# Kernel tuning notes

Measured on AMD Instinct MI355X. Metric: run time of the kernel, lower is better.

Reference implementation:

```python
import jax, jax.numpy as jnp
import numpy as np

DIM = 192
HEADS = 16
DIM_HEAD = 64
INNER = HEADS * DIM_HEAD  # 1024
B, N = 8, 1024


def setup_inputs() -> dict:
    key = jax.random.key(0)
    ks = jax.random.split(key, 8)
    x = jax.random.normal(ks[0], (B, N, DIM), dtype=jnp.float32)
    shift = jax.random.normal(ks[1], (B, 1, DIM), dtype=jnp.float32)
    scale = jax.random.normal(ks[2], (B, 1, DIM), dtype=jnp.float32)
    norm_w = jnp.ones((DIM,), dtype=jnp.float32)
    norm_b = jnp.zeros((DIM,), dtype=jnp.float32)
    w_qkv = jax.random.normal(ks[3], (DIM, 3 * INNER), dtype=jnp.float32) * (DIM ** -0.5)
    w_out = jax.random.normal(ks[4], (INNER, DIM), dtype=jnp.float32) * (INNER ** -0.5)
    b_out = jnp.zeros((DIM,), dtype=jnp.float32)
    return {"x": x, "shift": shift, "scale": scale, "norm_w": norm_w,
            "norm_b": norm_b, "w_qkv": w_qkv, "w_out": w_out, "b_out": b_out}


def _layernorm(x, w, b, eps=1e-5):
    mu = jnp.mean(x, axis=-1, keepdims=True)
    var = jnp.mean(jnp.square(x - mu), axis=-1, keepdims=True)
    return (x - mu) * jax.lax.rsqrt(var + eps) * w + b


def reference(x, shift, scale, norm_w, norm_b, w_qkv, w_out, b_out):
    h = _layernorm(x, norm_w, norm_b)
    h = h * (1.0 + scale) + shift  # adaLN modulation, broadcast over tokens
    qkv = h @ w_qkv  # [B, N, 3*INNER]
    q, k, v = jnp.split(qkv, 3, axis=-1)
    # [B, N, INNER] -> [B, H, N, Dh]
    def split_heads(t):
        return t.reshape(B, N, HEADS, DIM_HEAD).transpose(0, 2, 1, 3)
    q, k, v = split_heads(q), split_heads(k), split_heads(v)
    scores = jnp.einsum('bhnd,bhmd->bhnm', q, k) * (DIM_HEAD ** -0.5)
    attn = jax.nn.softmax(scores, axis=-1)
    out = jnp.einsum('bhnm,bhmd->bhnd', attn, v)  # [B, H, N, Dh]
    out = out.transpose(0, 2, 1, 3).reshape(B, N, INNER)
    return out @ w_out + b_out
```

## Files before the change

kernel.cpp:

```cpp
#include <hip/hip_runtime.h>

#define DIM 192
#define NB 8
#define NTOK 1024
#define HEADS 16
#define DH 64
#define INNER 1024
#define ROWS (NB * NTOK)

typedef __bf16 bf16x8 __attribute__((ext_vector_type(8)));
typedef float f32x4 __attribute__((ext_vector_type(4)));
typedef float f32x16 __attribute__((ext_vector_type(16)));
typedef unsigned int u32x4 __attribute__((ext_vector_type(4)));

__device__ inline unsigned short f2bf(float f) {
    union { float f; unsigned u; } v; v.f = f;
    unsigned r = v.u + 0x7FFF + ((v.u >> 16) & 1);
    return (unsigned short)(r >> 16);
}

__device__ inline unsigned pk2(float a, float b) {
    __bf16 x = (__bf16)a, y = (__bf16)b;
    unsigned short ux = __builtin_bit_cast(unsigned short, x);
    unsigned short uy = __builtin_bit_cast(unsigned short, y);
    return (unsigned)ux | ((unsigned)uy << 16);
}

__device__ inline size_t fragIdx(int row, int k, int depth) {
    return ((size_t)(row >> 5) * ((size_t)depth * 4) +
            (size_t)(((k >> 4) * 2 + ((k >> 3) & 1)) * 32 + (row & 31))) * 8 + (k & 7);
}

__global__ __launch_bounds__(256) void k_pre(
    const float* __restrict__ x, const float* __restrict__ shift,
    const float* __restrict__ scale, const float* __restrict__ nw,
    const float* __restrict__ nb, const float* __restrict__ wqkv,
    const float* __restrict__ wout,
    unsigned short* __restrict__ hF, unsigned short* __restrict__ wF,
    unsigned short* __restrict__ woF) {
    int bid = blockIdx.x;
    if (bid < 2048) {
        int row = bid * 4 + (threadIdx.x >> 6);
        int lane = threadIdx.x & 63;
        const float* xr = x + row * DIM;
        float v0 = xr[lane], v1 = xr[lane + 64], v2 = xr[lane + 128];
        float s = v0 + v1 + v2;
        #pragma unroll
        for (int m = 1; m < 64; m <<= 1) s += __shfl_xor(s, m);
        float mean = s * (1.0f / DIM);
        float d0 = v0 - mean, d1 = v1 - mean, d2 = v2 - mean;
        float q = d0 * d0 + d1 * d1 + d2 * d2;
        #pragma unroll
        for (int m = 1; m < 64; m <<= 1) q += __shfl_xor(q, m);
        float rs = rsqrtf(q * (1.0f / DIM) + 1e-5f);
        int b = row >> 10;
        float vv[3] = {v0, v1, v2};
        #pragma unroll
        for (int i = 0; i < 3; i++) {
            int d = lane + 64 * i;
            float val = (vv[i] - mean) * rs * nw[d] + nb[d];
            val = val * (1.0f + scale[b * DIM + d]) + shift[b * DIM + d];
            hF[fragIdx(row, d, DIM)] = f2bf(val);
        }
    } else if (bid < 4352) {
        int idx = (bid - 2048) * 256 + threadIdx.x;
        int k = idx / 3072, c = idx % 3072;
        wF[fragIdx(c, k, DIM)] = f2bf(wqkv[idx]);
    } else {
        int idx = (bid - 4352) * 256 + threadIdx.x;
        int k = idx / 192, c = idx % 192;
        woF[fragIdx(c, k, INNER)] = f2bf(wout[idx]);
    }
}

__global__ __launch_bounds__(256, 3) void k_qkv(
    const unsigned short* __restrict__ hF, const unsigned short* __restrict__ wF,
    unsigned short* __restrict__ qmF, unsigned short* __restrict__ kmF,
    unsigned short* __restrict__ vtF) {
    const float QSC = 0.125f * 1.4426950408889634f;
    int tid = threadIdx.x;
    int wave = tid >> 6, lane = tid & 63;
    int l31 = lane & 31, hi = lane >> 5;
    int c0 = blockIdx.x * 64 + (wave >> 1) * 32;
    int typ = c0 >> 10;
    int hd  = (c0 & 1023) >> 6;
    int coff = c0 & 32;

    const unsigned short* Ab = wF + (size_t)(c0 >> 5) * 768 * 8;
    bf16x8 af[12];
    #pragma unroll
    for (int kc = 0; kc < 12; kc++)
        af[kc] = *(const bf16x8*)(Ab + ((kc * 2 + hi) * 32 + l31) * 8);

    #pragma unroll
    for (int ns = 0; ns < 2; ns++) {
        int n0 = blockIdx.y * 128 + (wave & 1) * 64 + ns * 32;
        const unsigned short* Bb = hF + (size_t)(n0 >> 5) * 768 * 8;
        f32x16 acc0, acc1;
        #pragma unroll
        for (int r = 0; r < 16; r++) { acc0[r] = 0.f; acc1[r] = 0.f; }
        if (typ < 2) {
            #pragma unroll
            for (int kc = 0; kc < 6; kc++) {
                bf16x8 bf0 = *(const bf16x8*)(Bb + (((2 * kc) * 2 + hi) * 32 + l31) * 8);
                bf16x8 bf1 = *(const bf16x8*)(Bb + (((2 * kc + 1) * 2 + hi) * 32 + l31) * 8);
                acc0 = __builtin_amdgcn_mfma_f32_32x32x16_bf16(af[2 * kc], bf0, acc0, 0, 0, 0);
                acc1 = __builtin_amdgcn_mfma_f32_32x32x16_bf16(af[2 * kc + 1], bf1, acc1, 0, 0, 0);
            }
        } else {
            #pragma unroll
            for (int kc = 0; kc < 6; kc++) {
                bf16x8 bf0 = *(const bf16x8*)(Bb + (((2 * kc) * 2 + hi) * 32 + l31) * 8);
                bf16x8 bf1 = *(const bf16x8*)(Bb + (((2 * kc + 1) * 2 + hi) * 32 + l31) * 8);
                acc0 = __builtin_amdgcn_mfma_f32_32x32x16_bf16(bf0, af[2 * kc], acc0, 0, 0, 0);
                acc1 = __builtin_amdgcn_mfma_f32_32x32x16_bf16(bf1, af[2 * kc + 1], acc1, 0, 0, 0);
            }
        }
        f32x16 acc;
        #pragma unroll
        for (int r = 0; r < 16; r++) acc[r] = acc0[r] + acc1[r];

        int bb = n0 >> 10, nm = n0 & 1023;
        int tt = nm >> 6;
        unsigned short* base;
        if (typ == 0) base = qmF + (size_t)(bb * 16 + hd) * 65536;
        else if (typ == 1) base = kmF + (size_t)(bb * 16 + hd) * 65536;
        else base = vtF + (size_t)(bb * 16 + hd) * 65536;

        if (typ < 2) {
            float sc = (typ == 0) ? QSC : 1.0f;
            int rowgrp = (nm >> 5) & 1;
            #pragma unroll
            for (int rg = 0; rg < 4; rg++) {
                int ob = coff + rg * 8;
                int g = (rowgrp * 4 + (ob >> 4)) * 2 + ((ob >> 3) & 1);
                uint2 val;
                val.x = pk2(acc[rg * 4 + 0] * sc, acc[rg * 4 + 1] * sc);
                val.y = pk2(acc[rg * 4 + 2] * sc, acc[rg * 4 + 3] * sc);
                *(uint2*)(base + (tt * 16 + g) * 256 + l31 * 8 + hi * 4) = val;
            }
        } else {
            int drg = coff >> 5;
            #pragma unroll
            for (int rg = 0; rg < 4; rg++) {
                int nb2 = (nm & 32) + rg * 8;
                int g = (drg * 4 + (nb2 >> 4)) * 2 + ((nb2 >> 3) & 1);
                uint2 val;
                val.x = pk2(acc[rg * 4 + 0], acc[rg * 4 + 1]);
                val.y = pk2(acc[rg * 4 + 2], acc[rg * 4 + 3]);
                *(uint2*)(base + (tt * 16 + g) * 256 + l31 * 8 + hi * 4) = val;
            }
        }
    }
}

__global__ __launch_bounds__(256, 3) void k_attn(
    const unsigned short* __restrict__ qmF, const unsigned short* __restrict__ kmF,
    const unsigned short* __restrict__ vtF, unsigned short* __restrict__ attnF) {
    int tid = threadIdx.x;
    int wave = tid >> 6, lane = tid & 63;
    int l31 = lane & 31, hi = lane >> 5;
    int bh = blockIdx.x, qt = blockIdx.y;
    int qbase = qt * 128 + wave * 32;
    const unsigned short* Qb = qmF + (size_t)bh * 65536;
    const unsigned short* Kb = kmF + (size_t)bh * 65536;
    const unsigned short* Vb = vtF + (size_t)bh * 65536;

    int tq = qbase >> 6, rq = (qbase >> 5) & 1;
    bf16x8 qf[4];
    #pragma unroll
    for (int c = 0; c < 4; c++)
        qf[c] = *(const bf16x8*)(Qb + (tq * 16 + (rq * 4 + c) * 2 + hi) * 256 + l31 * 8);

    float lsum = 0.f;
    f32x16 accO[2];
    #pragma unroll
    for (int r = 0; r < 16; r++) { accO[0][r] = 0.f; accO[1][r] = 0.f; }

    auto ldKf = [&](int t, int rowgrp, int c) -> bf16x8 {
        return *(const bf16x8*)(Kb + (t * 16 + (rowgrp * 4 + c) * 2 + hi) * 256 + l31 * 8);
    };
    auto ldVf = [&](int t, int dt, int nc) -> bf16x8 {
        return *(const bf16x8*)(Vb + (t * 16 + (dt * 4 + nc) * 2 + hi) * 256 + l31 * 8);
    };
    auto packP = [&](const f32x16& P, bf16x8& w0, bf16x8& w1) {
        u32x4 A, B;
        {
            auto r0 = __builtin_amdgcn_permlane32_swap(pk2(P[0], P[1]), pk2(P[4], P[5]), false, false);
            auto r1 = __builtin_amdgcn_permlane32_swap(pk2(P[2], P[3]), pk2(P[6], P[7]), false, false);
            A[0] = r0[0]; A[1] = r1[0]; A[2] = r0[1]; A[3] = r1[1];
        }
        {
            auto r0 = __builtin_amdgcn_permlane32_swap(pk2(P[8], P[9]), pk2(P[12], P[13]), false, false);
            auto r1 = __builtin_amdgcn_permlane32_swap(pk2(P[10], P[11]), pk2(P[14], P[15]), false, false);
            B[0] = r0[0]; B[1] = r1[0]; B[2] = r0[1]; B[3] = r1[1];
        }
        w0 = __builtin_bit_cast(bf16x8, A);
        w1 = __builtin_bit_cast(bf16x8, B);
    };
    auto tsum = [](const f32x16& P) -> float {
        float s0 = (P[0] + P[1]) + (P[2] + P[3]);
        float s1 = (P[4] + P[5]) + (P[6] + P[7]);
        float s2 = (P[8] + P[9]) + (P[10] + P[11]);
        float s3 = (P[12] + P[13]) + (P[14] + P[15]);
        return (s0 + s1) + (s2 + s3);
    };

    bf16x8 pw[4];

    {
        f32x16 C0, C1;
        #pragma unroll
        for (int r = 0; r < 16; r++) { C0[r] = 0.f; C1[r] = 0.f; }
        #pragma unroll
        for (int c = 0; c < 4; c++) {
            C0 = __builtin_amdgcn_mfma_f32_32x32x16_bf16(ldKf(0, 0, c), qf[c], C0, 0, 0, 0);
            C1 = __builtin_amdgcn_mfma_f32_32x32x16_bf16(ldKf(0, 1, c), qf[c], C1, 0, 0, 0);
        }
        #pragma unroll
        for (int r = 0; r < 16; r++) {
            C0[r] = __builtin_amdgcn_exp2f(C0[r]);
            C1[r] = __builtin_amdgcn_exp2f(C1[r]);
        }
        lsum += tsum(C0) + tsum(C1);
        packP(C0, pw[0], pw[1]);
        packP(C1, pw[2], pw[3]);
    }

    for (int t = 1; t < 16; t++) {
        f32x16 C0, C1;
        #pragma unroll
        for (int r = 0; r < 16; r++) { C0[r] = 0.f; C1[r] = 0.f; }
        #pragma unroll
        for (int c = 0; c < 4; c++) {
            C0 = __builtin_amdgcn_mfma_f32_32x32x16_bf16(ldKf(t, 0, c), qf[c], C0, 0, 0, 0);
            C1 = __builtin_amdgcn_mfma_f32_32x32x16_bf16(ldKf(t, 1, c), qf[c], C1, 0, 0, 0);
        }
        #pragma unroll
        for (int dt = 0; dt < 2; dt++) {
            #pragma unroll
            for (int nc = 0; nc < 4; nc++) {
                accO[dt] = __builtin_amdgcn_mfma_f32_32x32x16_bf16(
                    ldVf(t - 1, dt, nc), pw[nc], accO[dt], 0, 0, 0);
            }
        }

        #pragma unroll
        for (int r = 0; r < 16; r++) {
            C0[r] = __builtin_amdgcn_exp2f(C0[r]);
            C1[r] = __builtin_amdgcn_exp2f(C1[r]);
        }
        lsum += tsum(C0) + tsum(C1);
        packP(C0, pw[0], pw[1]);
        packP(C1, pw[2], pw[3]);
    }

    #pragma unroll
    for (int dt = 0; dt < 2; dt++) {
        #pragma unroll
        for (int nc = 0; nc < 4; nc++) {
            accO[dt] = __builtin_amdgcn_mfma_f32_32x32x16_bf16(
                ldVf(15, dt, nc), pw[nc], accO[dt], 0, 0, 0);
        }
    }

    float inv = 1.0f / (lsum + __shfl_xor(lsum, 32));
    int b = bh >> 4, hd = bh & 15;
    int rowblk = b * 32 + qt * 4 + wave;
    #pragma unroll
    for (int dt = 0; dt < 2; dt++)
        #pragma unroll
        for (int rg = 0; rg < 4; rg++) {
            int g = (hd * 4 + dt * 2 + (rg >> 1)) * 2 + (rg & 1);
            uint2 val;
            val.x = pk2(accO[dt][rg * 4 + 0] * inv, accO[dt][rg * 4 + 1] * inv);
            val.y = pk2(accO[dt][rg * 4 + 2] * inv, accO[dt][rg * 4 + 3] * inv);
            *(uint2*)((char*)attnF + ((size_t)rowblk * 4096 + g * 32 + l31) * 16 + hi * 8) = val;
        }
}

__global__ __launch_bounds__(192, 2) void k_out(
    const unsigned short* __restrict__ attnF, const unsigned short* __restrict__ woF,
    const float* __restrict__ bias, float* __restrict__ out) {
    int wave = threadIdx.x >> 6, lane = threadIdx.x & 63;
    int l31 = lane & 31, hi = lane >> 5;
    int W = blockIdx.x * 3 + wave;
    int nb = W / 6, cb = W % 6;
    const unsigned short* A = attnF + (size_t)nb * 4096 * 8;
    const unsigned short* B = woF + (size_t)cb * 4096 * 8;

    f32x16 acc0, acc1;
    #pragma unroll
    for (int r = 0; r < 16; r++) { acc0[r] = 0.f; acc1[r] = 0.f; }
    #pragma unroll 8
    for (int kc = 0; kc < 32; kc++) {
        bf16x8 a0 = *(const bf16x8*)(A + (((2 * kc) * 2 + hi) * 32 + l31) * 8);
        bf16x8 b0 = *(const bf16x8*)(B + (((2 * kc) * 2 + hi) * 32 + l31) * 8);
        bf16x8 a1 = *(const bf16x8*)(A + (((2 * kc + 1) * 2 + hi) * 32 + l31) * 8);
        bf16x8 b1 = *(const bf16x8*)(B + (((2 * kc + 1) * 2 + hi) * 32 + l31) * 8);
        acc0 = __builtin_amdgcn_mfma_f32_32x32x16_bf16(a0, b0, acc0, 0, 0, 0);
        acc1 = __builtin_amdgcn_mfma_f32_32x32x16_bf16(a1, b1, acc1, 0, 0, 0);
    }
    float bi = bias[cb * 32 + l31];
    #pragma unroll
    for (int r = 0; r < 16; r++) {
        int n = nb * 32 + (r & 3) + 8 * (r >> 2) + 4 * hi;
        out[(size_t)n * DIM + cb * 32 + l31] = acc0[r] + acc1[r] + bi;
    }
}

extern "C" void kernel_launch(void* const* d_in, const int* in_sizes, int n_in,
                              void* d_out, int out_size, void* d_ws, size_t ws_size,
                              hipStream_t stream) {
    const float* x     = (const float*)d_in[0];
    const float* shift = (const float*)d_in[1];
    const float* scale = (const float*)d_in[2];
    const float* nw    = (const float*)d_in[3];
    const float* nbv   = (const float*)d_in[4];
    const float* wqkv  = (const float*)d_in[5];
    const float* wout  = (const float*)d_in[6];
    const float* bout  = (const float*)d_in[7];
    float* out = (float*)d_out;

    char* ws = (char*)d_ws;
    unsigned short* hF    = (unsigned short*)(ws + 0);
    unsigned short* wF    = (unsigned short*)(ws + 3145728);
    unsigned short* woF   = (unsigned short*)(ws + 3145728 + 1179648);
    unsigned short* qmF   = (unsigned short*)(ws + 4718592);
    unsigned short* kmF   = (unsigned short*)(ws + 4718592 + 16777216);
    unsigned short* vtF   = (unsigned short*)(ws + 4718592 + 2 * 16777216);
    unsigned short* attnF = (unsigned short*)(ws + 4718592 + 3 * 16777216);

    k_pre<<<dim3(5120), dim3(256), 0, stream>>>(x, shift, scale, nw, nbv, wqkv, wout, hF, wF, woF);
    k_qkv<<<dim3(48, 64), dim3(256), 0, stream>>>(hF, wF, qmF, kmF, vtF);
    k_attn<<<dim3(128, 8), dim3(256), 0, stream>>>(qmF, kmF, vtF, attnF);
    k_out<<<dim3(512), dim3(192), 0, stream>>>(attnF, woF, bout, out);
}
```

Before: 90.01 us.

## Split attention KV range across two wave groups and combine via shared memory

Doubles the attention block to 512 threads, with each group of four waves processing half of the key/value tiles for the same query rows. The partial output accumulators and row sums from the second half are written to LDS and added by the first half before normalization and store. This is split-K style parallelism meant to shorten the serial per-wave loop and raise occupancy, at the cost of an LDS round trip, a barrier, and higher launch-bound pressure on registers (512,6). Since there is no running-max softmax, the partial sums combine by simple addition.

Result: slower. 349.1 us (+287.9%).

```diff
diff --git a/kernel.cpp b/kernel.cpp
--- a/kernel.cpp
+++ b/kernel.cpp
@@ -154,14 +154,18 @@
     }
 }
 
-__global__ __launch_bounds__(256, 3) void k_attn(
+__global__ __launch_bounds__(512, 6) void k_attn(
     const unsigned short* __restrict__ qmF, const unsigned short* __restrict__ kmF,
     const unsigned short* __restrict__ vtF, unsigned short* __restrict__ attnF) {
+    __shared__ float combo[4][64][33];
     int tid = threadIdx.x;
     int wave = tid >> 6, lane = tid & 63;
     int l31 = lane & 31, hi = lane >> 5;
     int bh = blockIdx.x, qt = blockIdx.y;
-    int qbase = qt * 128 + wave * 32;
+    int qc = wave & 3;
+    int kvh = wave >> 2;
+    int qbase = qt * 128 + qc * 32;
+    int tbase = kvh * 8;
     const unsigned short* Qb = qmF + (size_t)bh * 65536;
     const unsigned short* Kb = kmF + (size_t)bh * 65536;
     const unsigned short* Vb = vtF + (size_t)bh * 65536;
@@ -214,8 +218,8 @@
         for (int r = 0; r < 16; r++) { C0[r] = 0.f; C1[r] = 0.f; }
         #pragma unroll
         for (int c = 0; c < 4; c++) {
-            C0 = __builtin_amdgcn_mfma_f32_32x32x16_bf16(ldKf(0, 0, c), qf[c], C0, 0, 0, 0);
-            C1 = __builtin_amdgcn_mfma_f32_32x32x16_bf16(ldKf(0, 1, c), qf[c], C1, 0, 0, 0);
+            C0 = __builtin_amdgcn_mfma_f32_32x32x16_bf16(ldKf(tbase, 0, c), qf[c], C0, 0, 0, 0);
+            C1 = __builtin_amdgcn_mfma_f32_32x32x16_bf16(ldKf(tbase, 1, c), qf[c], C1, 0, 0, 0);
         }
         #pragma unroll
         for (int r = 0; r < 16; r++) {
@@ -227,7 +231,8 @@
         packP(C1, pw[2], pw[3]);
     }
 
-    for (int t = 1; t < 16; t++) {
+    for (int i = 1; i < 8; i++) {
+        int t = tbase + i;
         f32x16 C0, C1;
         #pragma unroll
         for (int r = 0; r < 16; r++) { C0[r] = 0.f; C1[r] = 0.f; }
@@ -244,7 +249,6 @@
                     ldVf(t - 1, dt, nc), pw[nc], accO[dt], 0, 0, 0);
             }
         }
-
         #pragma unroll
         for (int r = 0; r < 16; r++) {
             C0[r] = __builtin_amdgcn_exp2f(C0[r]);
@@ -260,23 +264,41 @@
         #pragma unroll
         for (int nc = 0; nc < 4; nc++) {
             accO[dt] = __builtin_amdgcn_mfma_f32_32x32x16_bf16(
-                ldVf(15, dt, nc), pw[nc], accO[dt], 0, 0, 0);
-        }
-    }
-
-    float inv = 1.0f / (lsum + __shfl_xor(lsum, 32));
-    int b = bh >> 4, hd = bh & 15;
-    int rowblk = b * 32 + qt * 4 + wave;
-    #pragma unroll
-    for (int dt = 0; dt < 2; dt++)
-        #pragma unroll
-        for (int rg = 0; rg < 4; rg++) {
-            int g = (hd * 4 + dt * 2 + (rg >> 1)) * 2 + (rg & 1);
-            uint2 val;
-            val.x = pk2(accO[dt][rg * 4 + 0] * inv, accO[dt][rg * 4 + 1] * inv);
-            val.y = pk2(accO[dt][rg * 4 + 2] * inv, accO[dt][rg * 4 + 3] * inv);
-            *(uint2*)((char*)attnF + ((size_t)rowblk * 4096 + g * 32 + l31) * 16 + hi * 8) = val;
-        }
+                ldVf(tbase + 7, dt, nc), pw[nc], accO[dt], 0, 0, 0);
+        }
+    }
+
+    if (kvh == 1) {
+        #pragma unroll
+        for (int dt = 0; dt < 2; dt++)
+            #pragma unroll
+            for (int r = 0; r < 16; r++)
+                combo[qc][lane][dt * 16 + r] = accO[dt][r];
+        combo[qc][lane][32] = lsum;
+    }
+    __syncthreads();
+    if (kvh == 0) {
+        #pragma unroll
+        for (int dt = 0; dt < 2; dt++)
+            #pragma unroll
+            for (int r = 0; r < 16; r++)
+                accO[dt][r] += combo[qc][lane][dt * 16 + r];
+        lsum += combo[qc][lane][32];
+
+        float inv = 1.0f / (lsum + __shfl_xor(lsum, 32));
+        int b = bh >> 4, hd = bh & 15;
+        int rowblk = b * 32 + qt * 4 + qc;
+        #pragma unroll
+        for (int dt = 0; dt < 2; dt++)
+            #pragma unroll
+            for (int rg = 0; rg < 4; rg++) {
+                int g = (hd * 4 + dt * 2 + (rg >> 1)) * 2 + (rg & 1);
+                uint2 val;
+                val.x = pk2(accO[dt][rg * 4 + 0] * inv, accO[dt][rg * 4 + 1] * inv);
+                val.y = pk2(accO[dt][rg * 4 + 2] * inv, accO[dt][rg * 4 + 3] * inv);
+                *(uint2*)((char*)attnF + ((size_t)rowblk * 4096 + g * 32 + l31) * 16 + hi * 8) = val;
+            }
+    }
 }
 
 __global__ __launch_bounds__(192, 2) void k_out(
@@ -333,6 +355,6 @@
 
     k_pre<<<dim3(5120), dim3(256), 0, stream>>>(x, shift, scale, nw, nbv, wqkv, wout, hF, wF, woF);
     k_qkv<<<dim3(48, 64), dim3(256), 0, stream>>>(hF, wF, qmF, kmF, vtF);
-    k_attn<<<dim3(128, 8), dim3(256), 0, stream>>>(qmF, kmF, vtF, attnF);
+    k_attn<<<dim3(128, 8), dim3(512), 0, stream>>>(qmF, kmF, vtF, attnF);
     k_out<<<dim3(512), dim3(192), 0, stream>>>(attnF, woF, bout, out);
 }
```
